# Performance work log

Hardware: AMD Instinct MI355X
Metric: run time of the kernel (lower is better)

The kernel has to match this reference:

```python
import jax, jax.numpy as jnp
import numpy as np

N, S, T, D = 8, 2048, 2048, 1024


def setup_inputs() -> dict:
    key0 = jax.random.key(0)
    ks = jax.random.split(key0, 6)
    scale = 1.0 / np.sqrt(D).astype(np.float32)
    query = jax.random.normal(ks[0], (N, S, D), dtype=jnp.float32)
    key = jax.random.normal(ks[1], (N, T, D), dtype=jnp.float32)
    value = jax.random.normal(ks[2], (N, T, D), dtype=jnp.float32)
    # nn.Linear(D, D, bias=False) weights, shape [out, in]
    Wq = jax.random.normal(ks[3], (D, D), dtype=jnp.float32) * scale
    Wk = jax.random.normal(ks[4], (D, D), dtype=jnp.float32) * scale
    Wv = jax.random.normal(ks[5], (D, D), dtype=jnp.float32) * scale
    # causal mask: 1 on/below diagonal, 0 above (zeros become -inf additively)
    attn_mask = jnp.tril(jnp.ones((S, T), dtype=jnp.float32))
    return {"key": key, "query": query, "value": value,
            "Wq": Wq, "Wk": Wk, "Wv": Wv, "attn_mask": attn_mask}


def reference(key, query, value, Wq, Wk, Wv, attn_mask):
    d = query.shape[-1]
    q = query @ Wq.T              # [N,S,D]
    k = key @ Wk.T                # [N,T,D]
    v = value @ Wv.T              # [N,T,D]
    scores = jnp.einsum('nsd,ntd->nst', q, k)          # [N,S,T]
    # masked_fill(mask==0, -inf) then ADD the (nonzero) mask values
    additive = jnp.where(attn_mask == 0, -jnp.inf, attn_mask)
    scores = scores + additive                          # broadcast [S,T] -> [N,S,T]
    # NOTE: torch code divides by D**(-0.5), i.e. multiplies by sqrt(D). Faithful.
    attn = jax.nn.softmax(scores * jnp.sqrt(jnp.float32(d)), axis=-1)
    return jnp.einsum('nst,ntd->nsd', attn, v)          # [N,S,D]
```

## Files before the change

kernel.cpp:

```cpp
#include <hip/hip_runtime.h>
#include <hip/hip_bf16.h>


typedef __attribute__((ext_vector_type(4))) float f32x4;
typedef __attribute__((ext_vector_type(8))) short bf16x8;
typedef __attribute__((ext_vector_type(4))) short s16x4;

#define DEVI __device__ __forceinline__

DEVI unsigned short f2bf(float x) {
  union { float f; unsigned u; } v; v.f = x;
  unsigned r = v.u + 0x7FFFu + ((v.u >> 16) & 1u);
  return (unsigned short)(r >> 16);
}
DEVI float bf2f(unsigned short b) {
  union { float f; unsigned u; } v; v.u = ((unsigned)b) << 16;
  return v.f;
}

DEVI void gload16(const void* g, void* l) {
#if __has_builtin(__builtin_amdgcn_global_load_lds)
  typedef __attribute__((address_space(1))) const unsigned int* gas_u32;
  typedef __attribute__((address_space(3))) unsigned int* las_u32;
  __builtin_amdgcn_global_load_lds(
      (gas_u32)(unsigned long long)g,
      (las_u32)(unsigned int)(unsigned long long)l, 16, 0, 0);
#else
  *(bf16x8*)l = *(const bf16x8*)g;
#endif
}

DEVI int xcd_swizzle(int bid, int nwg) {
  if (nwg & 7) return bid;
  int cpx = nwg >> 3;
  return (bid & 7) * cpx + (bid >> 3);
}

#define WAITBAR(N) asm volatile("s_waitcnt vmcnt(" #N ")\ns_barrier" ::: "memory")
#define BAR()      asm volatile("s_barrier" ::: "memory")

DEVI void stage_pair(const unsigned short* __restrict__ s0, long long rs0,
                     const unsigned short* __restrict__ s1, long long rs1,
                     short* lds, int tid) {
#pragma unroll
  for (int it = 0; it < 4; ++it) {
    int ii = it * 256 + tid;
    int r = ii >> 3;
    int c8 = (ii & 7) ^ (r & 7);
    const unsigned short* src = (c8 < 4)
        ? s0 + (long long)r * rs0 + (c8 & 3) * 8
        : s1 + (long long)r * rs1 + (c8 & 3) * 8;
    gload16(src, &lds[ii * 8]);
  }
}

constexpr int NB = 8, SS = 2048, TT = 2048, DD = 1024;
constexpr long long TILE_E = 16384;

__global__ __launch_bounds__(256) void split_hl_k(
    const float* __restrict__ in, unsigned short* __restrict__ hi,
    unsigned short* __restrict__ lo, long long n4)
{
  long long i = (long long)blockIdx.x * 256 + threadIdx.x;
  long long stride = (long long)gridDim.x * 256;
  for (; i < n4; i += stride) {
    f32x4 v = ((const f32x4*)in)[i];
    s16x4 h, l;
#pragma unroll
    for (int e = 0; e < 4; ++e) {
      unsigned short hh = f2bf(v[e]);
      h[e] = (short)hh;
      l[e] = (short)f2bf(v[e] - bf2f(hh));
    }
    ((s16x4*)hi)[i] = h;
    ((s16x4*)lo)[i] = l;
  }
}

__global__ __launch_bounds__(256) void split_h_k(
    const float* __restrict__ in, unsigned short* __restrict__ hi, long long n4)
{
  long long i = (long long)blockIdx.x * 256 + threadIdx.x;
  long long stride = (long long)gridDim.x * 256;
  for (; i < n4; i += stride) {
    f32x4 v = ((const f32x4*)in)[i];
    s16x4 h;
#pragma unroll
    for (int e = 0; e < 4; ++e) h[e] = (short)f2bf(v[e]);
    ((s16x4*)hi)[i] = h;
  }
}

template<int NMFMA, bool SPLIT_OUT>
__global__ __launch_bounds__(256, 2) void gemm_bt(
    const unsigned short* __restrict__ Ah_g, const unsigned short* __restrict__ Al_g,
    const unsigned short* __restrict__ Bh_g, const unsigned short* __restrict__ Bl_g,
    unsigned short* __restrict__ Chi, unsigned short* __restrict__ Clo,
    int Nn, int K,
    long long aStride, long long bStride, long long cStride,
    int tilesM, int tilesN)
{
  constexpr int HALF = (NMFMA == 3) ? 16384 : 8192;
  __shared__ short lds[2 * HALF];

  int tid = threadIdx.x;
  int lane = tid & 63, wid = tid >> 6;
  int wr = wid >> 1, wc = wid & 1;
  int l15 = lane & 15, lq = lane >> 4;

  int wg = xcd_swizzle(blockIdx.x, gridDim.x);
  int tilesM2 = tilesM >> 1;
  int tilesPer = tilesM2 * tilesN;
  int b = wg / tilesPer;
  int rem = wg % tilesPer;
  int mt2 = rem / tilesN, nt = rem % tilesN;

  const unsigned short* Bgh = Bh_g + (long long)b * bStride + (long long)nt * 128 * K;
  const unsigned short* Bgl = (NMFMA == 3) ? Bl_g + (long long)b * bStride + (long long)nt * 128 * K : nullptr;

  for (int hm = 0; hm < 2; ++hm) {
    int mt = mt2 + hm * tilesM2;
    const unsigned short* Agh = Ah_g + (long long)b * aStride + (long long)mt * 128 * K;
    const unsigned short* Agl = (NMFMA == 3) ? Al_g + (long long)b * aStride + (long long)mt * 128 * K : nullptr;

    f32x4 acc[4][4];
#pragma unroll
    for (int i = 0; i < 4; ++i)
#pragma unroll
      for (int j = 0; j < 4; ++j) acc[i][j] = (f32x4){0.f, 0.f, 0.f, 0.f};

    auto stage = [&](int t, int h) {
      int k0 = t * 32;
      if constexpr (NMFMA == 3) {
        stage_pair(Agh + k0, K, Agl + k0, K, lds + h * HALF, tid);
        stage_pair(Bgh + k0, K, Bgl + k0, K, lds + h * HALF + 8192, tid);
      } else {
        stage_pair(Agh + k0, K, Bgh + k0, K, lds + h * HALF, tid);
      }
    };
    auto compute = [&](int h) {
      __builtin_amdgcn_s_setprio(1);
      if constexpr (NMFMA == 3) {
        const short* U = lds + h * HALF;
        const short* V = U + 8192;
        bf16x8 afh[4], afl[4], bfh[4], bfl[4];
#pragma unroll
        for (int i = 0; i < 4; ++i) {
          int ra = wr * 64 + i * 16 + l15;
          int sa = (ra & 7) << 4;
          afh[i] = *(const bf16x8*)(&U[((ra * 128 + lq * 16) ^ sa) >> 1]);
          afl[i] = *(const bf16x8*)(&U[((ra * 128 + 64 + lq * 16) ^ sa) >> 1]);
          int rb = wc * 64 + i * 16 + l15;
          int sb = (rb & 7) << 4;
          bfh[i] = *(const bf16x8*)(&V[((rb * 128 + lq * 16) ^ sb) >> 1]);
          bfl[i] = *(const bf16x8*)(&V[((rb * 128 + 64 + lq * 16) ^ sb) >> 1]);
        }
#pragma unroll
        for (int i = 0; i < 4; ++i)
#pragma unroll
          for (int j = 0; j < 4; ++j) {
            acc[i][j] = __builtin_amdgcn_mfma_f32_16x16x32_bf16(afh[i], bfh[j], acc[i][j], 0, 0, 0);
            acc[i][j] = __builtin_amdgcn_mfma_f32_16x16x32_bf16(afh[i], bfl[j], acc[i][j], 0, 0, 0);
            acc[i][j] = __builtin_amdgcn_mfma_f32_16x16x32_bf16(afl[i], bfh[j], acc[i][j], 0, 0, 0);
          }
      } else {
        const short* W = lds + h * HALF;
        bf16x8 af[4], bfr[4];
#pragma unroll
        for (int i = 0; i < 4; ++i) {
          int ra = wr * 64 + i * 16 + l15;
          af[i] = *(const bf16x8*)(&W[((ra * 128 + lq * 16) ^ ((ra & 7) << 4)) >> 1]);
          int rb = wc * 64 + i * 16 + l15;
          bfr[i] = *(const bf16x8*)(&W[((rb * 128 + 64 + lq * 16) ^ ((rb & 7) << 4)) >> 1]);
        }
#pragma unroll
        for (int i = 0; i < 4; ++i)
#pragma unroll
          for (int j = 0; j < 4; ++j)
            acc[i][j] = __builtin_amdgcn_mfma_f32_16x16x32_bf16(af[i], bfr[j], acc[i][j], 0, 0, 0);
      }
      __builtin_amdgcn_s_setprio(0);
    };

    int NT = K >> 5;
    stage(0, 0);
    stage(1, 1);
    for (int t = 0; t < NT; ++t) {
      if (t < NT - 1) {
        if constexpr (NMFMA == 3) WAITBAR(8); else WAITBAR(4);
      } else {
        WAITBAR(0);
      }
      compute(t & 1);
      BAR();
      if (t + 2 < NT) stage(t + 2, t & 1);
    }

    unsigned short* ch = Chi + (long long)b * cStride;
    unsigned short* cl = SPLIT_OUT ? (Clo + (long long)b * cStride) : nullptr;
#pragma unroll
    for (int i = 0; i < 4; ++i)
#pragma unroll
      for (int j = 0; j < 4; ++j)
#pragma unroll
        for (int e = 0; e < 4; ++e) {
          int row = mt * 128 + wr * 64 + i * 16 + lq * 4 + e;
          int col = nt * 128 + wc * 64 + j * 16 + l15;
          float vv = acc[i][j][e];
          unsigned short h = f2bf(vv);
          ch[(long long)row * Nn + col] = h;
          if constexpr (SPLIT_OUT) cl[(long long)row * Nn + col] = f2bf(vv - bf2f(h));
        }
    BAR();
  }
}

__global__ __launch_bounds__(256, 2) void qk_bt(
    const unsigned short* __restrict__ qh, const unsigned short* __restrict__ ql,
    const unsigned short* __restrict__ kh, const unsigned short* __restrict__ kl,
    float* __restrict__ Sg)
{
  __shared__ short lds[2 * 16384];

  int tid = threadIdx.x;
  int lane = tid & 63, wid = tid >> 6;
  int wr = wid >> 1, wc = wid & 1;
  int l15 = lane & 15, lq = lane >> 4;

  int wg = xcd_swizzle(blockIdx.x, gridDim.x);
  int b = wg / 136;
  int idx = wg % 136;
  int st = (int)((sqrtf(8.f * (float)idx + 1.f) - 1.f) * 0.5f);
  while ((st + 1) * (st + 2) / 2 <= idx) ++st;
  while (st * (st + 1) / 2 > idx) --st;
  int tt = idx - st * (st + 1) / 2;

  const unsigned short* Agh = qh + (long long)b * SS * DD + (long long)st * 128 * DD;
  const unsigned short* Agl = ql + (long long)b * SS * DD + (long long)st * 128 * DD;
  const unsigned short* Bgh = kh + (long long)b * TT * DD + (long long)tt * 128 * DD;
  const unsigned short* Bgl = kl + (long long)b * TT * DD + (long long)tt * 128 * DD;

  f32x4 acc[4][4];
#pragma unroll
  for (int i = 0; i < 4; ++i)
#pragma unroll
    for (int j = 0; j < 4; ++j) acc[i][j] = (f32x4){0.f, 0.f, 0.f, 0.f};

  auto stage = [&](int t, int h) {
    int k0 = t * 32;
    stage_pair(Agh + k0, DD, Agl + k0, DD, lds + h * 16384, tid);
    stage_pair(Bgh + k0, DD, Bgl + k0, DD, lds + h * 16384 + 8192, tid);
  };
  auto compute = [&](int h) {
    __builtin_amdgcn_s_setprio(1);
    const short* U = lds + h * 16384;
    const short* V = U + 8192;
    bf16x8 afh[4], afl[4], bfh[4], bfl[4];
#pragma unroll
    for (int i = 0; i < 4; ++i) {
      int ra = wr * 64 + i * 16 + l15;
      int sa = (ra & 7) << 4;
      afh[i] = *(const bf16x8*)(&U[((ra * 128 + lq * 16) ^ sa) >> 1]);
      afl[i] = *(const bf16x8*)(&U[((ra * 128 + 64 + lq * 16) ^ sa) >> 1]);
      int rb = wc * 64 + i * 16 + l15;
      int sb = (rb & 7) << 4;
      bfh[i] = *(const bf16x8*)(&V[((rb * 128 + lq * 16) ^ sb) >> 1]);
      bfl[i] = *(const bf16x8*)(&V[((rb * 128 + 64 + lq * 16) ^ sb) >> 1]);
    }
#pragma unroll
    for (int i = 0; i < 4; ++i)
#pragma unroll
      for (int j = 0; j < 4; ++j) {
        acc[i][j] = __builtin_amdgcn_mfma_f32_16x16x32_bf16(afh[i], bfh[j], acc[i][j], 0, 0, 0);
        acc[i][j] = __builtin_amdgcn_mfma_f32_16x16x32_bf16(afh[i], bfl[j], acc[i][j], 0, 0, 0);
        acc[i][j] = __builtin_amdgcn_mfma_f32_16x16x32_bf16(afl[i], bfh[j], acc[i][j], 0, 0, 0);
      }
    __builtin_amdgcn_s_setprio(0);
  };

  stage(0, 0);
  stage(1, 1);
  for (int t = 0; t < 32; ++t) {
    if (t < 31) WAITBAR(8); else WAITBAR(0);
    compute(t & 1);
    BAR();
    if (t + 2 < 32) stage(t + 2, t & 1);
  }

  float* Sb = Sg + ((long long)b * 136 + idx) * TILE_E;
#pragma unroll
  for (int i = 0; i < 4; ++i)
#pragma unroll
    for (int j = 0; j < 4; ++j)
#pragma unroll
      for (int e = 0; e < 4; ++e) {
        int row = wr * 64 + i * 16 + lq * 4 + e;
        int col = wc * 64 + j * 16 + l15;
        Sb[(long long)row * 128 + col] = acc[i][j][e];
      }
}

__global__ __launch_bounds__(256) void softmax_kernel(float* __restrict__ Sg)
{
  __shared__ float red[8];
  int blk = blockIdx.x;
  int b = blk >> 11, s = blk & 2047;
  int st = s >> 7, r = s & 127;
  long long tri = (long long)st * (st + 1) / 2;
  const float* tb = Sg + ((long long)b * 136 + tri) * TILE_E + (long long)r * 128;

  int tid = threadIdx.x;
  int lane = tid & 63, wid = tid >> 6;

  int c0 = tid * 8;
  int tt = c0 >> 7, cc = c0 & 127;
  bool live = (c0 <= s);
  f32x4 v0 = {0.f, 0.f, 0.f, 0.f}, v1 = {0.f, 0.f, 0.f, 0.f};
  if (live) {
    const float* seg = tb + (long long)tt * TILE_E + cc;
    v0 = *(const f32x4*)seg;
    v1 = *(const f32x4*)(seg + 4);
  }

  float m = -3.0e38f;
#pragma unroll
  for (int e = 0; e < 4; ++e) {
    if (c0 + e <= s) m = fmaxf(m, v0[e]);
    if (c0 + 4 + e <= s) m = fmaxf(m, v1[e]);
  }
#pragma unroll
  for (int o = 32; o > 0; o >>= 1) m = fmaxf(m, __shfl_xor(m, o));
  if (lane == 0) red[wid] = m;
  __syncthreads();
  m = fmaxf(fmaxf(red[0], red[1]), fmaxf(red[2], red[3]));

  const float C = 46.16624130844683f;
  float p0[4], p1[4];
  float sum = 0.f;
#pragma unroll
  for (int e = 0; e < 4; ++e) {
    p0[e] = (c0 + e <= s) ? exp2f((v0[e] - m) * C) : 0.f;
    sum += p0[e];
    p1[e] = (c0 + 4 + e <= s) ? exp2f((v1[e] - m) * C) : 0.f;
    sum += p1[e];
  }
#pragma unroll
  for (int o = 32; o > 0; o >>= 1) sum += __shfl_xor(sum, o);
  if (lane == 0) red[4 + wid] = sum;
  __syncthreads();
  float inv = 1.f / (red[4] + red[5] + red[6] + red[7]);

  union { bf16x8 v; s16x4 h[2]; } w;
#pragma unroll
  for (int e = 0; e < 4; ++e) {
    w.h[0][e] = (short)f2bf(p0[e] * inv);
    w.h[1][e] = (short)f2bf(p1[e] * inv);
  }
  __syncthreads();
  if (c0 < (st + 1) * 128) {
    unsigned short* pw = (unsigned short*)Sg +
        (((long long)b * 136 + tri + tt) * TILE_E) * 2 + (long long)r * 256 + cc;
    *(bf16x8*)pw = w.v;
  }
}

__global__ __launch_bounds__(256, 2) void pv_bt(
    const unsigned short* __restrict__ P, const unsigned short* __restrict__ vT,
    float* __restrict__ Out)
{
  __shared__ short lds[2 * 8192];

  int tid = threadIdx.x;
  int lane = tid & 63, wid = tid >> 6;
  int wr = wid >> 1, wc = wid & 1;
  int l15 = lane & 15, lq = lane >> 4;

  int wg = xcd_swizzle(blockIdx.x, gridDim.x);
  int b = wg >> 7;
  int rem = wg & 127;
  int st = 15 - (rem >> 3);
  int dt = rem & 7;

  const unsigned short* Ps = P + ((long long)b * 136 + (long long)st * (st + 1) / 2) * (TILE_E * 2);
  const unsigned short* Vb = vT + (long long)b * DD * TT + (long long)dt * 128 * TT;
  int NT = (st + 1) * 4;

  f32x4 acc[4][4];
#pragma unroll
  for (int i = 0; i < 4; ++i)
#pragma unroll
    for (int j = 0; j < 4; ++j) acc[i][j] = (f32x4){0.f, 0.f, 0.f, 0.f};

  auto stage = [&](int t, int h) {
    int t0 = t * 32;
    const unsigned short* s0 = Ps + (long long)(t0 >> 7) * (TILE_E * 2) + (t0 & 127);
    stage_pair(s0, 256, Vb + t0, TT, lds + h * 8192, tid);
  };
  auto compute = [&](int h) {
    __builtin_amdgcn_s_setprio(1);
    const short* W = lds + h * 8192;
    bf16x8 af[4], bfr[4];
#pragma unroll
    for (int i = 0; i < 4; ++i) {
      int ra = wr * 64 + i * 16 + l15;
      af[i] = *(const bf16x8*)(&W[((ra * 128 + lq * 16) ^ ((ra & 7) << 4)) >> 1]);
      int rb = wc * 64 + i * 16 + l15;
      bfr[i] = *(const bf16x8*)(&W[((rb * 128 + 64 + lq * 16) ^ ((rb & 7) << 4)) >> 1]);
    }
#pragma unroll
    for (int i = 0; i < 4; ++i)
#pragma unroll
      for (int j = 0; j < 4; ++j)
        acc[i][j] = __builtin_amdgcn_mfma_f32_16x16x32_bf16(af[i], bfr[j], acc[i][j], 0, 0, 0);
    __builtin_amdgcn_s_setprio(0);
  };

  stage(0, 0);
  stage(1, 1);
  for (int t = 0; t < NT; ++t) {
    if (t < NT - 1) WAITBAR(4); else WAITBAR(0);
    compute(t & 1);
    BAR();
    if (t + 2 < NT) stage(t + 2, t & 1);
  }

  float* Ob = Out + (long long)b * SS * DD;
#pragma unroll
  for (int i = 0; i < 4; ++i)
#pragma unroll
    for (int j = 0; j < 4; ++j)
#pragma unroll
      for (int e = 0; e < 4; ++e) {
        int row = st * 128 + wr * 64 + i * 16 + lq * 4 + e;
        int col = dt * 128 + wc * 64 + j * 16 + l15;
        Ob[(long long)row * DD + col] = acc[i][j][e];
      }
}

extern "C" void kernel_launch(void* const* d_in, const int* in_sizes, int n_in,
                              void* d_out, int out_size, void* d_ws, size_t ws_size,
                              hipStream_t stream) {
  (void)in_sizes; (void)n_in; (void)out_size;
  const float* key   = (const float*)d_in[0];
  const float* query = (const float*)d_in[1];
  const float* value = (const float*)d_in[2];
  const float* Wq    = (const float*)d_in[3];
  const float* Wk    = (const float*)d_in[4];
  const float* Wv    = (const float*)d_in[5];
  float* Out = (float*)d_out;

  const long long SD = (long long)SS * DD;
  const long long DT = (long long)DD * TT;
  const long long WN = (long long)DD * DD;

  const unsigned long long PLANE_B  = (unsigned long long)SD * 2;
  const unsigned long long WPLANE_B = (unsigned long long)WN * 2;
  const unsigned long long SCORE_B  = 136ull * TILE_E * 4;

  auto need = [&](int g) -> unsigned long long {
    return 5ull * WPLANE_B + (unsigned long long)g * (SCORE_B + 5ull * PLANE_B);
  };
  int G = 1;
  for (int g : {8, 4, 2, 1}) if (ws_size >= need(g)) { G = g; break; }

  char* ws = (char*)d_ws;
  size_t off = 0;
  auto alloc = [&](unsigned long long bytes) { char* p = ws + off; off += bytes; return p; };

  unsigned short* wqh = (unsigned short*)alloc(WPLANE_B);
  unsigned short* wql = (unsigned short*)alloc(WPLANE_B);
  unsigned short* wkh = (unsigned short*)alloc(WPLANE_B);
  unsigned short* wkl = (unsigned short*)alloc(WPLANE_B);
  unsigned short* wvh = (unsigned short*)alloc(WPLANE_B);
  char* slab = alloc((unsigned long long)G * SCORE_B);
  unsigned short* qh  = (unsigned short*)alloc((unsigned long long)G * PLANE_B);
  unsigned short* ql  = (unsigned short*)alloc((unsigned long long)G * PLANE_B);
  unsigned short* kh  = (unsigned short*)alloc((unsigned long long)G * PLANE_B);
  unsigned short* kl  = (unsigned short*)alloc((unsigned long long)G * PLANE_B);
  unsigned short* vT  = (unsigned short*)alloc((unsigned long long)G * PLANE_B);

  unsigned short* iah = (unsigned short*)slab;
  unsigned short* ial = (unsigned short*)(slab + (unsigned long long)G * PLANE_B);
  float* Sg = (float*)slab;

  split_hl_k<<<512, 256, 0, stream>>>(Wq, wqh, wql, WN / 4);
  split_hl_k<<<512, 256, 0, stream>>>(Wk, wkh, wkl, WN / 4);
  split_h_k<<<512, 256, 0, stream>>>(Wv, wvh, WN / 4);

  for (int b0 = 0; b0 < NB; b0 += G) {
    long long n4 = (long long)G * SD / 4;
    split_hl_k<<<2048, 256, 0, stream>>>(query + (long long)b0 * SD, iah, ial, n4);
    gemm_bt<3, true><<<G * 64, 256, 0, stream>>>(
        iah, ial, wqh, wql, qh, ql, DD, DD, SD, 0, SD, 16, 8);
    split_hl_k<<<2048, 256, 0, stream>>>(key + (long long)b0 * SD, iah, ial, n4);
    gemm_bt<3, true><<<G * 64, 256, 0, stream>>>(
        iah, ial, wkh, wkl, kh, kl, DD, DD, SD, 0, SD, 16, 8);
    split_h_k<<<2048, 256, 0, stream>>>(value + (long long)b0 * SD, iah, n4);
    gemm_bt<1, false><<<G * 64, 256, 0, stream>>>(
        wvh, nullptr, iah, nullptr, vT, nullptr, TT, DD, 0, SD, DT, 8, 16);
    qk_bt<<<G * 136, 256, 0, stream>>>(qh, ql, kh, kl, Sg);
    softmax_kernel<<<G * SS, 256, 0, stream>>>(Sg);
    pv_bt<<<G * 128, 256, 0, stream>>>(
        (const unsigned short*)Sg, vT, Out + (long long)b0 * SD);
  }
}
```

Measured before the change: 538.8 us.

## Fold Wk into query projection via precomputed Wq^T·Wk to skip key GEMM

Computes a combined matrix M = Wk^T Wq (from transposed, hi/lo-split copies of both weights) once, then projects the query by M. The raw key is used directly as the K operand, so the per-batch key projection GEMM is removed. This trades one batched D×D GEMM per batch for a single small D×D×D GEMM plus a transpose-split pass. Precision may change slightly because the weight product is rounded before use.

```diff
diff --git a/kernel.cpp b/kernel.cpp
--- a/kernel.cpp
+++ b/kernel.cpp
@@ -88,6 +88,40 @@
 #pragma unroll
     for (int e = 0; e < 4; ++e) h[e] = (short)f2bf(v[e]);
     ((s16x4*)hi)[i] = h;
+  }
+}
+
+__global__ __launch_bounds__(256) void tsplit_k(
+    const float* __restrict__ W, unsigned short* __restrict__ Th,
+    unsigned short* __restrict__ Tl)
+{
+  __shared__ float t[64][68];
+  int bi = blockIdx.x & 15, bj = blockIdx.x >> 4;
+  int tid = threadIdx.x;
+  int lr = tid >> 2, lc4 = tid & 3;
+#pragma unroll
+  for (int q = 0; q < 4; ++q) {
+    int col = (lc4 + q * 4) * 4;
+    f32x4 v = *(const f32x4*)(W + (long long)(bj * 64 + lr) * DD + bi * 64 + col);
+    t[lr][col] = v[0]; t[lr][col + 1] = v[1];
+    t[lr][col + 2] = v[2]; t[lr][col + 3] = v[3];
+  }
+  __syncthreads();
+  int orow = tid >> 2, ch = tid & 3;
+#pragma unroll
+  for (int cc = 0; cc < 2; ++cc) {
+    int c0 = (ch + cc * 4) * 8;
+    bf16x8 h, l;
+#pragma unroll
+    for (int e = 0; e < 8; ++e) {
+      float v = t[c0 + e][orow];
+      unsigned short hh = f2bf(v);
+      h[e] = (short)hh;
+      l[e] = (short)f2bf(v - bf2f(hh));
+    }
+    long long o = (long long)(bi * 64 + orow) * DD + bj * 64 + c0;
+    *(bf16x8*)(Th + o) = h;
+    *(bf16x8*)(Tl + o) = l;
   }
 }
 
@@ -458,7 +492,7 @@
   const unsigned long long SCORE_B  = 136ull * TILE_E * 4;
 
   auto need = [&](int g) -> unsigned long long {
-    return 5ull * WPLANE_B + (unsigned long long)g * (SCORE_B + 5ull * PLANE_B);
+    return 3ull * WPLANE_B + (unsigned long long)g * (SCORE_B + 5ull * PLANE_B);
   };
   int G = 1;
   for (int g : {8, 4, 2, 1}) if (ws_size >= need(g)) { G = g; break; }
@@ -467,10 +501,8 @@
   size_t off = 0;
   auto alloc = [&](unsigned long long bytes) { char* p = ws + off; off += bytes; return p; };
 
-  unsigned short* wqh = (unsigned short*)alloc(WPLANE_B);
-  unsigned short* wql = (unsigned short*)alloc(WPLANE_B);
-  unsigned short* wkh = (unsigned short*)alloc(WPLANE_B);
-  unsigned short* wkl = (unsigned short*)alloc(WPLANE_B);
+  unsigned short* mph = (unsigned short*)alloc(WPLANE_B);
+  unsigned short* mpl = (unsigned short*)alloc(WPLANE_B);
   unsigned short* wvh = (unsigned short*)alloc(WPLANE_B);
   char* slab = alloc((unsigned long long)G * SCORE_B);
   unsigned short* qh  = (unsigned short*)alloc((unsigned long long)G * PLANE_B);
@@ -479,22 +511,27 @@
   unsigned short* kl  = (unsigned short*)alloc((unsigned long long)G * PLANE_B);
   unsigned short* vT  = (unsigned short*)alloc((unsigned long long)G * PLANE_B);
 
+  unsigned short* wqTh = (unsigned short*)slab;
+  unsigned short* wqTl = (unsigned short*)(slab + WPLANE_B);
+  unsigned short* wkTh = (unsigned short*)(slab + 2 * WPLANE_B);
+  unsigned short* wkTl = (unsigned short*)(slab + 3 * WPLANE_B);
+
   unsigned short* iah = (unsigned short*)slab;
   unsigned short* ial = (unsigned short*)(slab + (unsigned long long)G * PLANE_B);
   float* Sg = (float*)slab;
 
-  split_hl_k<<<512, 256, 0, stream>>>(Wq, wqh, wql, WN / 4);
-  split_hl_k<<<512, 256, 0, stream>>>(Wk, wkh, wkl, WN / 4);
+  tsplit_k<<<256, 256, 0, stream>>>(Wq, wqTh, wqTl);
+  tsplit_k<<<256, 256, 0, stream>>>(Wk, wkTh, wkTl);
   split_h_k<<<512, 256, 0, stream>>>(Wv, wvh, WN / 4);
+  gemm_bt<3, true><<<32, 256, 0, stream>>>(
+      wkTh, wkTl, wqTh, wqTl, mph, mpl, DD, DD, 0, 0, 0, 8, 8);
 
   for (int b0 = 0; b0 < NB; b0 += G) {
     long long n4 = (long long)G * SD / 4;
     split_hl_k<<<2048, 256, 0, stream>>>(query + (long long)b0 * SD, iah, ial, n4);
     gemm_bt<3, true><<<G * 64, 256, 0, stream>>>(
-        iah, ial, wqh, wql, qh, ql, DD, DD, SD, 0, SD, 16, 8);
-    split_hl_k<<<2048, 256, 0, stream>>>(key + (long long)b0 * SD, iah, ial, n4);
-    gemm_bt<3, true><<<G * 64, 256, 0, stream>>>(
-        iah, ial, wkh, wkl, kh, kl, DD, DD, SD, 0, SD, 16, 8);
+        iah, ial, mph, mpl, qh, ql, DD, DD, SD, 0, SD, 16, 8);
+    split_hl_k<<<2048, 256, 0, stream>>>(key + (long long)b0 * SD, kh, kl, n4);
     split_h_k<<<2048, 256, 0, stream>>>(value + (long long)b0 * SD, iah, n4);
     gemm_bt<1, false><<<G * 64, 256, 0, stream>>>(
         wvh, nullptr, iah, nullptr, vT, nullptr, TT, DD, 0, SD, DT, 8, 16);
```

New measurement: 494.5 us. 1.09x faster.
